# Kernel optimization log

Measured on AMD Instinct MI355X. Metric: run time of the kernel, lower is better.

Reference implementation:

```python
import jax, jax.numpy as jnp
import numpy as np

QN, QP = -8, 7  # signed 4-bit


def round_pass(x):
    # straight-through round (forward: round-half-even like torch.round)
    return x + jax.lax.stop_gradient(jnp.round(x) - x)


def setup_inputs() -> dict:
    key = jax.random.key(0)
    ks = jax.random.split(key, 9)
    B, S, D, H = 16, 1024, 768, 3072
    def unif(k, shape):
        return jax.random.uniform(k, shape, jnp.float32, 0.02, 0.1)
    return {
        "x0": jax.random.normal(ks[0], (B, S, D), jnp.float32),
        "w1": jax.random.normal(ks[1], (H, D), jnp.float32) * 0.02,
        "b1": jax.random.normal(ks[2], (H,), jnp.float32) * 0.02,
        "alpha_w1": unif(ks[3], (H,)),
        "alpha_a1": unif(ks[4], (D,)),
        "w2": jax.random.normal(ks[5], (D, H), jnp.float32) * 0.02,
        "b2": jax.random.normal(ks[6], (D,), jnp.float32) * 0.02,
        "alpha_w2": unif(ks[7], (D,)),
        "alpha_a2": unif(ks[8], (H,)),
    }


def _quant_act(x, alpha_a):
    # ActQ_v2: per-tensor (mean of kernel-wise alpha), signed int4
    a = alpha_a.mean()
    return round_pass(jnp.clip(x / a, QN, QP))


def _quant_w(w, alpha_w):
    # LinearQ_v2: per-output-channel alpha, shape [out, in]
    return round_pass(jnp.clip(w / alpha_w[:, None], QN, QP))


def reference(x0, w1, b1, alpha_w1, alpha_a1, w2, b2, alpha_w2, alpha_a2):
    # fc1: int4 act quant, int4 weight quant, integer matmul, dequant scale + bias
    xq = _quant_act(x0, alpha_a1)                       # [B,S,D] integer-valued
    wq1 = _quant_w(w1, alpha_w1)                        # [H,D] integer-valued
    x1 = jnp.einsum('bsd,hd->bsh', xq, wq1)             # int matmul (float carrier)
    x1 = x1 * alpha_w1 * alpha_a1.mean() + b1           # per-channel dequant + bias
    x1 = jax.nn.gelu(x1, approximate=False)             # nn.GELU (exact erf)
    x1 = jnp.clip(x1, -10.0, 10.0)
    # dropout p=0.0 -> identity
    # fc2
    hq = _quant_act(x1, alpha_a2)                       # [B,S,H]
    wq2 = _quant_w(w2, alpha_w2)                        # [D,H]
    x2 = jnp.einsum('bsh,dh->bsd', hq, wq2)
    x2 = x2 * alpha_w2 * alpha_a2.mean() + b2
    return x2
```

## Files before the change

### kernel.cpp

```cpp
#include <hip/hip_runtime.h>
#include <hip/hip_bf16.h>
#include <math.h>


typedef __attribute__((ext_vector_type(4))) int i32x4;

__device__ __forceinline__ void gload_lds16(const void* g, void* l) {
  __builtin_amdgcn_global_load_lds(
      (const __attribute__((address_space(1))) void*)g,
      (__attribute__((address_space(3))) void*)l, 16, 0, 0);
}

__device__ __forceinline__ int q4_i8(float x, float a) {
  float t = x / a;
  t = fminf(fmaxf(t, -8.0f), 7.0f);
  t = rintf(t);
  return (int)t;
}

__global__ void means_k(const float* __restrict__ v1, int n1,
                        const float* __restrict__ v2, int n2,
                        float* __restrict__ out) {
  const float* src = blockIdx.x ? v2 : v1;
  const int n = blockIdx.x ? n2 : n1;
  __shared__ double red[256];
  double s = 0.0;
  for (int i = threadIdx.x; i < n; i += 256) s += (double)src[i];
  red[threadIdx.x] = s;
  __syncthreads();
  for (int st = 128; st > 0; st >>= 1) {
    if (threadIdx.x < st) red[threadIdx.x] += red[threadIdx.x + st];
    __syncthreads();
  }
  if (threadIdx.x == 0) {
    float m = (float)(red[0] / (double)n);
    out[blockIdx.x] = m;
    if (blockIdx.x == 1) {
      out[2] = 1.0f / m;
      out[3] = 0.5f * (1.0f / m);
    }
  }
}

__global__ void quant_x_k(const float* __restrict__ x,
                          unsigned* __restrict__ xq,
                          const float* __restrict__ means, int n4) {
  int i = blockIdx.x * blockDim.x + threadIdx.x;
  if (i >= n4) return;
  const float a = means[0];
  float4 v = ((const float4*)x)[i];
  unsigned u = (q4_i8(v.x, a) & 0xFF) | ((q4_i8(v.y, a) & 0xFF) << 8) |
               ((q4_i8(v.z, a) & 0xFF) << 16) | ((q4_i8(v.w, a) & 0xFF) << 24);
  xq[i] = u;
}

__global__ void quant_w_k(const float* __restrict__ w,
                          const float* __restrict__ alpha,
                          unsigned* __restrict__ wq, int C, int n4) {
  int i = blockIdx.x * blockDim.x + threadIdx.x;
  if (i >= n4) return;
  int row = (i * 4) / C;
  const float a = alpha[row];
  float4 v = ((const float4*)w)[i];
  unsigned u = (q4_i8(v.x, a) & 0xFF) | ((q4_i8(v.y, a) & 0xFF) << 8) |
               ((q4_i8(v.z, a) & 0xFF) << 16) | ((q4_i8(v.w, a) & 0xFF) << 24);
  wq[i] = u;
}

template <int EPI>
__global__ __launch_bounds__(256, 4) void gemm_k(
    const signed char* __restrict__ A, const signed char* __restrict__ B,
    const float* __restrict__ alphaw, const float* __restrict__ bias,
    const float* __restrict__ means, signed char* __restrict__ out_b,
    float* __restrict__ out_f, int N, int K) {
  __shared__ __align__(16) signed char sA[128 * 128];
  __shared__ __align__(16) signed char sB[128 * 128];
  const int tid = threadIdx.x;
  const int w = tid >> 6;
  const int l = tid & 63;
  const int wm = w >> 1, wn = w & 1;
  const long bm0 = (long)blockIdx.y * 128;
  const long bn0 = (long)blockIdx.x * 128;

  i32x4 acc[4][4] = {};

  const int srow = l >> 3;
  const int scol = ((l & 7) * 16) ^ (srow << 4);
  const int rsw = (l & 7) << 4;

  for (int kt = 0; kt < K; kt += 128) {
    __syncthreads();
#pragma unroll
    for (int i = 0; i < 4; ++i) {
      const int c = w * 4 + i;
      const int row = c * 8 + srow;
      gload_lds16(A + (bm0 + row) * K + kt + scol, &sA[c * 1024]);
      gload_lds16(B + (bn0 + row) * K + kt + scol, &sB[c * 1024]);
    }
    __syncthreads();
#pragma unroll
    for (int kk = 0; kk < 2; ++kk) {
      const int kc = (kk * 64 + (l >> 4) * 16) ^ rsw;
      i32x4 af[4], bg[4];
#pragma unroll
      for (int m = 0; m < 4; ++m)
        af[m] = *(const i32x4*)&sA[(wm * 64 + m * 16 + (l & 15)) * 128 + kc];
#pragma unroll
      for (int n = 0; n < 4; ++n)
        bg[n] = *(const i32x4*)&sB[(wn * 64 + n * 16 + (l & 15)) * 128 + kc];
#pragma unroll
      for (int m = 0; m < 4; ++m)
#pragma unroll
        for (int n = 0; n < 4; ++n)
          acc[m][n] = __builtin_amdgcn_mfma_i32_16x16x64_i8(af[m], bg[n],
                                                            acc[m][n], 0, 0, 0);
    }
  }

  const float a1 = means[0];
  const float a2 = means[1];
  const float half_inv_a2 = means[3];

  float awc[4], bsc[4];
  const int cc0 = (int)bn0 + wn * 64 + (l & 15);
#pragma unroll
  for (int n = 0; n < 4; ++n) {
    awc[n] = alphaw[cc0 + n * 16];
    bsc[n] = bias[cc0 + n * 16];
  }

  const int r0 = (int)bm0 + wm * 64 + (l >> 4) * 4;

  if (EPI == 1) {
    float awa1[4];
#pragma unroll
    for (int n = 0; n < 4; ++n) awa1[n] = awc[n] * a1;
#pragma unroll
    for (int m = 0; m < 4; ++m) {
#pragma unroll
      for (int rg = 0; rg < 4; ++rg) {
        const int r = r0 + m * 16 + rg;
        signed char* prow = out_b + (size_t)r * N + cc0;
#pragma unroll
        for (int n = 0; n < 4; ++n) {
          const float f = (float)acc[m][n][rg];
          const float t = fmaf(f, awa1[n], bsc[n]);
          const float x = t * 0.70710678118654752f;
          const float az = fabsf(x);
          const float rr = __builtin_amdgcn_rcpf(fmaf(0.3275911f, az, 1.0f));
          float p = fmaf(rr, 1.061405429f, -1.453152027f);
          p = fmaf(rr, p, 1.421413741f);
          p = fmaf(rr, p, -0.284496736f);
          p = fmaf(rr, p, 0.254829592f);
          p = p * rr;
          const float e = __expf(-az * az);
          float er = fmaf(-p, e, 1.0f);
          er = copysignf(er, x);
          float qv = t * (1.0f + er) * half_inv_a2;
          qv = fminf(fmaxf(qv, -8.0f), 7.0f);
          qv = rintf(qv);
          prow[n * 16] = (signed char)(int)qv;
        }
      }
    }
  } else {
#pragma unroll
    for (int m = 0; m < 4; ++m) {
#pragma unroll
      for (int rg = 0; rg < 4; ++rg) {
        const int r = r0 + m * 16 + rg;
        float* prow = out_f + (size_t)r * N + cc0;
#pragma unroll
        for (int n = 0; n < 4; ++n) {
          const float f = (float)acc[m][n][rg];
          float t = __fmul_rn(f, awc[n]);
          t = __fmul_rn(t, a2);
          t = __fadd_rn(t, bsc[n]);
          prow[n * 16] = t;
        }
      }
    }
  }
}

extern "C" void kernel_launch(void* const* d_in, const int* in_sizes, int n_in,
                              void* d_out, int out_size, void* d_ws,
                              size_t ws_size, hipStream_t stream) {
  const float* x0 = (const float*)d_in[0];
  const float* w1 = (const float*)d_in[1];
  const float* b1 = (const float*)d_in[2];
  const float* aw1 = (const float*)d_in[3];
  const float* aa1 = (const float*)d_in[4];
  const float* w2 = (const float*)d_in[5];
  const float* b2 = (const float*)d_in[6];
  const float* aw2 = (const float*)d_in[7];
  const float* aa2 = (const float*)d_in[8];

  char* ws = (char*)d_ws;
  float* means = (float*)ws;
  signed char* xq = (signed char*)(ws + 256);
  signed char* wq1 = (signed char*)(ws + 12583168);
  signed char* wq2 = (signed char*)(ws + 14942464);
  signed char* hq = (signed char*)(ws + 17301760);

  means_k<<<2, 256, 0, stream>>>(aa1, 768, aa2, 3072, means);
  quant_x_k<<<12288, 256, 0, stream>>>(x0, (unsigned*)xq, means, 3145728);
  quant_w_k<<<2304, 256, 0, stream>>>(w1, aw1, (unsigned*)wq1, 768, 589824);
  quant_w_k<<<2304, 256, 0, stream>>>(w2, aw2, (unsigned*)wq2, 3072, 589824);
  dim3 g1(24, 128);
  gemm_k<1><<<g1, 256, 0, stream>>>(xq, wq1, aw1, b1, means, hq, nullptr, 3072,
                                    768);
  dim3 g2(6, 128);
  gemm_k<2><<<g2, 256, 0, stream>>>(hq, wq2, aw2, b2, means, nullptr,
                                    (float*)d_out, 768, 3072);
}
```

Baseline: 136.3 us.

## Double-buffer LDS tiles in int8 GEMM to overlap loads with MFMA

```diff
diff --git a/kernel.cpp b/kernel.cpp
--- a/kernel.cpp
+++ b/kernel.cpp
@@ -68,13 +68,15 @@
 }
 
 template <int EPI>
-__global__ __launch_bounds__(256, 4) void gemm_k(
+__global__ __launch_bounds__(256, 2) void gemm_k(
     const signed char* __restrict__ A, const signed char* __restrict__ B,
     const float* __restrict__ alphaw, const float* __restrict__ bias,
     const float* __restrict__ means, signed char* __restrict__ out_b,
     float* __restrict__ out_f, int N, int K) {
-  __shared__ __align__(16) signed char sA[128 * 128];
-  __shared__ __align__(16) signed char sB[128 * 128];
+  __shared__ __align__(16) signed char sA0[128 * 128];
+  __shared__ __align__(16) signed char sB0[128 * 128];
+  __shared__ __align__(16) signed char sA1[128 * 128];
+  __shared__ __align__(16) signed char sB1[128 * 128];
   const int tid = threadIdx.x;
   const int w = tid >> 6;
   const int l = tid & 63;
@@ -88,26 +90,27 @@
   const int scol = ((l & 7) * 16) ^ (srow << 4);
   const int rsw = (l & 7) << 4;
 
-  for (int kt = 0; kt < K; kt += 128) {
-    __syncthreads();
+  const signed char* gA = A + (bm0 + (w * 4) * 8 + srow) * (long)K + scol;
+  const signed char* gB = B + (bn0 + (w * 4) * 8 + srow) * (long)K + scol;
+
+  auto STAGE = [&](signed char* dA, signed char* dB, int kt) {
 #pragma unroll
     for (int i = 0; i < 4; ++i) {
-      const int c = w * 4 + i;
-      const int row = c * 8 + srow;
-      gload_lds16(A + (bm0 + row) * K + kt + scol, &sA[c * 1024]);
-      gload_lds16(B + (bn0 + row) * K + kt + scol, &sB[c * 1024]);
-    }
-    __syncthreads();
+      gload_lds16(gA + (long)i * 8 * K + kt, dA + (w * 4 + i) * 1024);
+      gload_lds16(gB + (long)i * 8 * K + kt, dB + (w * 4 + i) * 1024);
+    }
+  };
+  auto COMPUTE = [&](const signed char* pA, const signed char* pB) {
 #pragma unroll
     for (int kk = 0; kk < 2; ++kk) {
       const int kc = (kk * 64 + (l >> 4) * 16) ^ rsw;
       i32x4 af[4], bg[4];
 #pragma unroll
       for (int m = 0; m < 4; ++m)
-        af[m] = *(const i32x4*)&sA[(wm * 64 + m * 16 + (l & 15)) * 128 + kc];
+        af[m] = *(const i32x4*)&pA[(wm * 64 + m * 16 + (l & 15)) * 128 + kc];
 #pragma unroll
       for (int n = 0; n < 4; ++n)
-        bg[n] = *(const i32x4*)&sB[(wn * 64 + n * 16 + (l & 15)) * 128 + kc];
+        bg[n] = *(const i32x4*)&pB[(wn * 64 + n * 16 + (l & 15)) * 128 + kc];
 #pragma unroll
       for (int m = 0; m < 4; ++m)
 #pragma unroll
@@ -115,6 +118,18 @@
           acc[m][n] = __builtin_amdgcn_mfma_i32_16x16x64_i8(af[m], bg[n],
                                                             acc[m][n], 0, 0, 0);
     }
+  };
+
+  const int nt = K >> 7;
+  STAGE(sA0, sB0, 0);
+  __syncthreads();
+  for (int t = 0; t < nt; t += 2) {
+    if (t + 1 < nt) STAGE(sA1, sB1, (t + 1) << 7);
+    COMPUTE(sA0, sB0);
+    __syncthreads();
+    if (t + 2 < nt) STAGE(sA0, sB0, (t + 2) << 7);
+    COMPUTE(sA1, sB1);
+    __syncthreads();
   }
 
   const float a1 = means[0];
```

New measurement: 149.5 us. 9.7% more time.
